# Kernel optimization log

Measured on AMD Instinct MI355X. Metric: run time of the kernel, lower is better.

## Reference

```python
import jax, jax.numpy as jnp
import numpy as np

N_HEADS = 16

def _rope_tables(L, head_dim, dtype):
    inv_freq = 1.0 / (10000.0 ** (jnp.arange(0, head_dim, 2, dtype=jnp.float32) / head_dim))
    t = jnp.arange(L, dtype=jnp.float32)
    freqs = jnp.outer(t, inv_freq)            # [L, head_dim/2]
    emb = jnp.concatenate([freqs, freqs], -1)  # [L, head_dim]
    return jnp.cos(emb).astype(dtype), jnp.sin(emb).astype(dtype)

def _apply_rope(x, cos, sin):
    # x: [B, L, H, hd]; cos/sin: [1, L, 1, hd]
    half = x.shape[-1] // 2
    x1, x2 = x[..., :half], x[..., half:]
    x_rot = jnp.concatenate([-x2, x1], -1)
    return x * cos + x_rot * sin

def setup_inputs() -> dict:
    key = jax.random.key(0)
    ks = jax.random.split(key, 5)
    D = 1024
    s = 0.02
    return {
        "x": jax.random.normal(ks[0], (4, 2048, D), jnp.float32),
        "w_qkv": jax.random.normal(ks[1], (3 * D, D), jnp.float32) * s,
        "b_qkv": jax.random.normal(ks[2], (3 * D,), jnp.float32) * s,
        "w_out": jax.random.normal(ks[3], (D, D), jnp.float32) * s,
        "b_out": jax.random.normal(ks[4], (D,), jnp.float32) * s,
    }

def reference(x, w_qkv, b_qkv, w_out, b_out):
    B, L, D = x.shape
    H = N_HEADS
    hd = D // H
    scale = hd ** -0.5
    qkv = (x @ w_qkv.T + b_qkv).reshape(B, L, 3, H, hd)
    q, k, v = qkv[:, :, 0], qkv[:, :, 1], qkv[:, :, 2]  # [B,L,H,hd]
    cos, sin = _rope_tables(L, hd, x.dtype)
    cos = cos[None, :, None, :]
    sin = sin[None, :, None, :]
    q = _apply_rope(q, cos, sin)
    k = _apply_rope(k, cos, sin)
    # [B,H,L,L] scores, non-causal softmax
    attn = jnp.einsum('blhd,bmhd->bhlm', q, k) * scale
    attn = jax.nn.softmax(attn, axis=-1)
    out = jnp.einsum('bhlm,bmhd->blhd', attn, v).reshape(B, L, D)
    return out @ w_out.T + b_out
```

## Files before the change

kernel.cpp:

```cpp
#include <hip/hip_runtime.h>
#include <stdint.h>

typedef __attribute__((ext_vector_type(4))) float f32x4;
typedef __attribute__((ext_vector_type(8))) short bf16x8;
typedef __attribute__((ext_vector_type(4))) short s16x4;
typedef __attribute__((ext_vector_type(4))) float fp32x4;

#define QSCALE 0.18033688f

__device__ __forceinline__ short f2bf(float f) {
    union { float f; unsigned u; } v; v.f = f;
    unsigned u = v.u;
    unsigned r = u + 0x7fffu + ((u >> 16) & 1u);
    return (short)(r >> 16);
}
__device__ __forceinline__ unsigned cvtpk(float a, float b) {
    unsigned r;
    asm("v_cvt_pk_bf16_f32 %0, %1, %2" : "=v"(r) : "v"(a), "v"(b));
    return r;
}

__device__ __forceinline__ void gld_lds16(const void* g, void* l) {
    __builtin_amdgcn_global_load_lds(
        (const __attribute__((address_space(1))) unsigned int*)(uintptr_t)g,
        (__attribute__((address_space(3))) unsigned int*)(uintptr_t)l,
        16, 0, 0);
}

__global__ __launch_bounds__(256) void cast_kernel(const float* __restrict__ in,
                                                   short* __restrict__ out, int n) {
    int idx = (blockIdx.x * 256 + threadIdx.x) * 8;
    if (idx >= n) return;
    fp32x4 a = *(const fp32x4*)&in[idx];
    fp32x4 b = *(const fp32x4*)&in[idx + 4];
    union { unsigned w[4]; bf16x8 v; } u;
    u.w[0] = cvtpk(a[0], a[1]); u.w[1] = cvtpk(a[2], a[3]);
    u.w[2] = cvtpk(b[0], b[1]); u.w[3] = cvtpk(b[2], b[3]);
    *(bf16x8*)&out[idx] = u.v;
}

__global__ __launch_bounds__(256) void rope_table_kernel(float* __restrict__ tab) {
    int idx = blockIdx.x * 256 + threadIdx.x;
    int l = idx >> 5, d = idx & 31;
    float inv = expf(-(float)d / 32.f * logf(10000.f));
    float ang = (float)l * inv;
    tab[idx * 2 + 0] = cosf(ang);
    tab[idx * 2 + 1] = sinf(ang);
}

template<int MODE>
__global__ __launch_bounds__(256) void gemm_bt(const short* __restrict__ A,
                                               const short* __restrict__ B,
                                               const float* __restrict__ bias,
                                               void* __restrict__ Cout,
                                               short* __restrict__ VTout,
                                               const float* __restrict__ tab,
                                               int M, int N, int K) {
    __shared__ short As[128 * 64];
    __shared__ short Bs[128 * 64];
    const int tid = threadIdx.x;
    const int lane = tid & 63, wave = tid >> 6;
    const int i15 = lane & 15, g = lane >> 4;
    const int wr = wave >> 1, wc = wave & 1;
    const int m0 = blockIdx.y * 128, n0 = blockIdx.x * 128;

    const int xr3 = i15 & 3, xb2 = (i15 >> 2) & 1;
    const int cLo = g ^ xr3;
    const int aoff0 = (wr * 64 + i15) * 64 + (xb2 * 4 + cLo) * 8;
    const int aoff1 = (wr * 64 + i15) * 64 + ((1 ^ xb2) * 4 + cLo) * 8;
    const int boff0 = (wc * 64 + i15) * 64 + (xb2 * 4 + cLo) * 8;
    const int boff1 = (wc * 64 + i15) * 64 + ((1 ^ xb2) * 4 + cLo) * 8;

    f32x4 acc[4][4] = {};

    for (int k0 = 0; k0 < K; k0 += 64) {
        __syncthreads();
#pragma unroll
        for (int r = 0; r < 4; ++r) {
            const int gx = r * 256 + tid;
            const int row = gx >> 3, s = gx & 7;
            const int ss = s ^ (row & 7);
            gld_lds16(A + (size_t)(m0 + row) * K + k0 + ss * 8,
                      As + (size_t)(r * 256 + wave * 64) * 8);
            gld_lds16(B + (size_t)(n0 + row) * K + k0 + ss * 8,
                      Bs + (size_t)(r * 256 + wave * 64) * 8);
        }
        __syncthreads();
#pragma unroll
        for (int ks = 0; ks < 2; ++ks) {
            const int ao = ks ? aoff1 : aoff0, bo = ks ? boff1 : boff0;
            bf16x8 af[4], bfr[4];
#pragma unroll
            for (int m = 0; m < 4; ++m) af[m] = *(const bf16x8*)&As[ao + m * 1024];
#pragma unroll
            for (int n = 0; n < 4; ++n) bfr[n] = *(const bf16x8*)&Bs[bo + n * 1024];
#pragma unroll
            for (int m = 0; m < 4; ++m)
#pragma unroll
                for (int n = 0; n < 4; ++n)
                    acc[m][n] = __builtin_amdgcn_mfma_f32_16x16x32_bf16(af[m], bfr[n], acc[m][n], 0, 0, 0);
        }
    }

    if (MODE == 0) {
#pragma unroll
        for (int m = 0; m < 4; ++m)
#pragma unroll
            for (int n = 0; n < 4; ++n) {
                int col = n0 + wc * 64 + n * 16 + i15;
                float bcol = bias[col];
#pragma unroll
                for (int j = 0; j < 4; ++j) {
                    int row = m0 + wr * 64 + m * 16 + g * 4 + j;
                    ((float*)Cout)[(size_t)row * N + col] = acc[m][n][j] + bcol;
                }
            }
    } else {
        const int sec = n0 >> 10;
        if (sec < 2) {
            const float qs = (sec == 0) ? QSCALE : 1.0f;
            short* out = (short*)Cout;
#pragma unroll
            for (int m = 0; m < 4; ++m) {
#pragma unroll
                for (int pp = 0; pp < 2; ++pp) {
                    int d = pp * 16 + i15;
                    int collo = n0 + wc * 64 + pp * 16 + i15;
                    float blo = bias[collo], bhi = bias[collo + 32];
#pragma unroll
                    for (int j = 0; j < 4; ++j) {
                        int row = m0 + wr * 64 + m * 16 + g * 4 + j;
                        int l = row & 2047;
                        float2 cs = *(const float2*)&tab[(l * 32 + d) * 2];
                        float x1 = acc[m][pp][j] + blo;
                        float x2 = acc[m][pp + 2][j] + bhi;
                        out[(size_t)row * 3072 + collo]      = f2bf((x1 * cs.x - x2 * cs.y) * qs);
                        out[(size_t)row * 3072 + collo + 32] = f2bf((x2 * cs.x + x1 * cs.y) * qs);
                    }
                }
            }
        } else {
#pragma unroll
            for (int m = 0; m < 4; ++m) {
                int rbase = m0 + wr * 64 + m * 16 + g * 4;
                int lbase = rbase & 2047, bidx = rbase >> 11;
#pragma unroll
                for (int n = 0; n < 4; ++n) {
                    int vcol = (n0 - 2048) + wc * 64 + n * 16 + i15;
                    int h = vcol >> 6, d = vcol & 63;
                    float bb = bias[n0 + wc * 64 + n * 16 + i15];
                    union { unsigned w[2]; s16x4 v; } u;
                    u.w[0] = cvtpk(acc[m][n][0] + bb, acc[m][n][1] + bb);
                    u.w[1] = cvtpk(acc[m][n][2] + bb, acc[m][n][3] + bb);
                    *(s16x4*)&VTout[((size_t)(bidx * 16 + h) * 64 + d) * 2048 + lbase] = u.v;
                }
            }
        }
    }
}

__global__ __launch_bounds__(512, 8) void attn_kernel(const short* __restrict__ qkv,
                                                      const short* __restrict__ VT,
                                                      short* __restrict__ O) {
    __shared__ short Ks[2][64 * 64];
    __shared__ short Vs[2][64 * 64];
    int orig = blockIdx.x;
    int xcd = orig & 7, idx = orig >> 3;
    int bh = xcd * 8 + (idx >> 4), qt = idx & 15;
    int b = bh >> 4, h = bh & 15;
    int tid = threadIdx.x, lane = tid & 63, wave = tid >> 6;
    int i15 = lane & 15, g = lane >> 4;
    int q0 = qt * 128;

    size_t qrow = (size_t)(b * 2048 + q0 + wave * 16 + i15);
    bf16x8 qf[2];
    qf[0] = *(const bf16x8*)&qkv[qrow * 3072 + h * 64 + 0  + g * 8];
    qf[1] = *(const bf16x8*)&qkv[qrow * 3072 + h * 64 + 32 + g * 8];

    bf16x8 onesf;
#pragma unroll
    for (int e = 0; e < 8; ++e) onesf[e] = (short)0x3F80;

    {
    }
    const int srow = tid >> 3, ss8 = (tid & 7) ^ (srow & 7);
    const int sprow = (srow & 0x23) | ((srow & 0x10) >> 2) | ((srow & 0x0C) << 1);
    const short* kp = qkv + (size_t)(b * 2048) * 3072 + 1024 + h * 64
                      + (size_t)sprow * 3072 + ss8 * 8;
    const short* vp = VT + (size_t)bh * 64 * 2048 + (size_t)srow * 2048 + ss8 * 8;

    const int xr3 = i15 & 3, xb2 = (i15 >> 2) & 1;
    const int cLo = g ^ xr3;
    const int o0 = i15 * 64 + (xb2 * 4 + cLo) * 8;
    const int o1 = i15 * 64 + ((1 ^ xb2) * 4 + cLo) * 8;

    f32x4 acc_o[4] = {};
    f32x4 acc_l = {0.f, 0.f, 0.f, 0.f};

#define STAGE(bk, bv)                                        \
    do {                                                     \
        gld_lds16(kp, (bk) + wave * 512);                    \
        gld_lds16(vp, (bv) + wave * 512);                    \
        kp += 64 * 3072;                                     \
        vp += 64;                                            \
    } while (0)

    STAGE(Ks[0], Vs[0]);

    for (int t = 0; t < 32; ++t) {
        const int cur = t & 1;
        if (t > 0) {
            __builtin_amdgcn_s_barrier();
            __builtin_amdgcn_sched_barrier(0);
        }
        if (t + 1 < 32) {
            STAGE(Ks[cur ^ 1], Vs[cur ^ 1]);
            asm volatile("s_waitcnt vmcnt(2)" ::: "memory");
        } else {
            asm volatile("s_waitcnt vmcnt(0)" ::: "memory");
        }
        __builtin_amdgcn_s_barrier();
        __builtin_amdgcn_sched_barrier(0);

        const short* ks = Ks[cur];
        const short* vs = Vs[cur];

        f32x4 sa[4] = {};
        __builtin_amdgcn_s_setprio(1);
#pragma unroll
        for (int kb = 0; kb < 2; ++kb) {
            const int ko = kb ? o1 : o0;
#pragma unroll
            for (int jb = 0; jb < 4; ++jb) {
                bf16x8 kf = *(const bf16x8*)&ks[ko + jb * 1024];
                sa[jb] = __builtin_amdgcn_mfma_f32_16x16x32_bf16(kf, qf[kb], sa[jb], 0, 0, 0);
            }
        }
        __builtin_amdgcn_s_setprio(0);

        float p[4][4];
#pragma unroll
        for (int jb = 0; jb < 4; ++jb)
#pragma unroll
            for (int r = 0; r < 4; ++r)
                p[jb][r] = __builtin_amdgcn_exp2f(sa[jb][r]);

        bf16x8 pf[2];
#pragma unroll
        for (int kb = 0; kb < 2; ++kb) {
            union { unsigned w[4]; bf16x8 v; } u;
            u.w[0] = cvtpk(p[2 * kb][0],     p[2 * kb][1]);
            u.w[1] = cvtpk(p[2 * kb][2],     p[2 * kb][3]);
            u.w[2] = cvtpk(p[2 * kb + 1][0], p[2 * kb + 1][1]);
            u.w[3] = cvtpk(p[2 * kb + 1][2], p[2 * kb + 1][3]);
            pf[kb] = u.v;
        }

        __builtin_amdgcn_s_setprio(1);
#pragma unroll
        for (int db = 0; db < 4; ++db) {
#pragma unroll
            for (int kb = 0; kb < 2; ++kb) {
                bf16x8 vf = *(const bf16x8*)&vs[(kb ? o1 : o0) + db * 1024];
                acc_o[db] = __builtin_amdgcn_mfma_f32_16x16x32_bf16(pf[kb], vf, acc_o[db], 0, 0, 0);
            }
        }
        acc_l = __builtin_amdgcn_mfma_f32_16x16x32_bf16(pf[0], onesf, acc_l, 0, 0, 0);
        acc_l = __builtin_amdgcn_mfma_f32_16x16x32_bf16(pf[1], onesf, acc_l, 0, 0, 0);
        __builtin_amdgcn_s_setprio(0);
    }
#undef STAGE

    float linv4[4];
#pragma unroll
    for (int r = 0; r < 4; ++r) linv4[r] = 1.f / acc_l[r];
#pragma unroll
    for (int db = 0; db < 4; ++db) {
        int ocol = h * 64 + db * 16 + i15;
#pragma unroll
        for (int r = 0; r < 4; ++r) {
            int orow = b * 2048 + q0 + wave * 16 + g * 4 + r;
            O[(size_t)orow * 1024 + ocol] = f2bf(acc_o[db][r] * linv4[r]);
        }
    }
}

extern "C" void kernel_launch(void* const* d_in, const int* in_sizes, int n_in,
                              void* d_out, int out_size, void* d_ws, size_t ws_size,
                              hipStream_t stream) {
    const float* x     = (const float*)d_in[0];
    const float* w_qkv = (const float*)d_in[1];
    const float* b_qkv = (const float*)d_in[2];
    const float* w_out = (const float*)d_in[3];
    const float* b_out = (const float*)d_in[4];

    char* ws = (char*)d_ws;
    short* qkvb = (short*)(ws);
    short* xb   = (short*)(ws + 50331648);
    short* wqb  = (short*)(ws + 67108864);
    short* wob  = (short*)(ws + 73400320);
    short* VT   = (short*)(ws + 75497472);
    float* rt   = (float*)(ws + 92274688);
    short* Ob   = xb;

    cast_kernel<<<4096, 256, 0, stream>>>(x, xb, 8388608);
    cast_kernel<<<1536, 256, 0, stream>>>(w_qkv, wqb, 3145728);
    cast_kernel<<<512, 256, 0, stream>>>(w_out, wob, 1048576);
    rope_table_kernel<<<256, 256, 0, stream>>>(rt);

    gemm_bt<1><<<dim3(24, 64), 256, 0, stream>>>(xb, wqb, b_qkv, qkvb, VT, rt, 8192, 3072, 1024);
    attn_kernel<<<1024, 512, 0, stream>>>(qkvb, VT, Ob);
    gemm_bt<0><<<dim3(8, 64), 256, 0, stream>>>(Ob, wob, b_out, d_out, nullptr, nullptr, 8192, 1024, 1024);
}
```

Before: 192.2 us.

## Pipeline GEMM with triple-buffered LDS, 256x128 tiles, and XCD-aware block swizzle

Rewrites the bf16 GEMM main loop to use a three-slot LDS ring with asynchronous global-to-LDS prefetch two tiles ahead. Loads are split into halves that are interleaved with MFMA phases, using s_setprio and explicit waitcnt/barriers in place of full __syncthreads around each tile. Block tiles grow to 256x128 with 512 threads, and block IDs are remapped across the 8 XCDs for cache locality. The aim is to hide global-load latency behind MFMA work and cut the number of blocks and barriers. The cost is more LDS per block (144KB), which limits occupancy, and fewer blocks, which risks tail imbalance on the small output GEMM.

```diff
diff --git a/kernel.cpp b/kernel.cpp
--- a/kernel.cpp
+++ b/kernel.cpp
@@ -49,20 +49,25 @@
 }
 
 template<int MODE>
-__global__ __launch_bounds__(256) void gemm_bt(const short* __restrict__ A,
-                                               const short* __restrict__ B,
-                                               const float* __restrict__ bias,
-                                               void* __restrict__ Cout,
-                                               short* __restrict__ VTout,
-                                               const float* __restrict__ tab,
-                                               int M, int N, int K) {
-    __shared__ short As[128 * 64];
-    __shared__ short Bs[128 * 64];
+__global__ __launch_bounds__(512, 2) void gemm_bt(const short* __restrict__ A,
+                                                  const short* __restrict__ B,
+                                                  const float* __restrict__ bias,
+                                                  void* __restrict__ Cout,
+                                                  short* __restrict__ VTout,
+                                                  const float* __restrict__ tab,
+                                                  int M, int N, int K) {
+    __shared__ short lds[3 * 24576];
     const int tid = threadIdx.x;
     const int lane = tid & 63, wave = tid >> 6;
     const int i15 = lane & 15, g = lane >> 4;
     const int wr = wave >> 1, wc = wave & 1;
-    const int m0 = blockIdx.y * 128, n0 = blockIdx.x * 128;
+
+    const int nbx = gridDim.x;
+    const int nwg = nbx * gridDim.y;
+    int bid = blockIdx.y * nbx + blockIdx.x;
+    int sw = (bid & 7) * (nwg >> 3) + (bid >> 3);
+    const int m0 = (sw / nbx) * 256;
+    const int n0 = (sw % nbx) * 128;
 
     const int xr3 = i15 & 3, xb2 = (i15 >> 2) & 1;
     const int cLo = g ^ xr3;
@@ -71,36 +76,87 @@
     const int boff0 = (wc * 64 + i15) * 64 + (xb2 * 4 + cLo) * 8;
     const int boff1 = (wc * 64 + i15) * 64 + ((1 ^ xb2) * 4 + cLo) * 8;
 
+    const int srow = tid >> 3;
+    const int ss = (tid & 7) ^ (srow & 7);
+    const short* a0 = A + (size_t)(m0 + srow) * K + ss * 8;
+    const short* a1 = a0 + (size_t)64 * K;
+    const short* a2 = a0 + (size_t)128 * K;
+    const short* a3 = a0 + (size_t)192 * K;
+    const short* b0 = B + (size_t)(n0 + srow) * K + ss * 8;
+    const short* b1 = b0 + (size_t)64 * K;
+
+#define ST_A(slot, r, p) do { gld_lds16(p, lds + (slot) * 24576 + ((r) * 512 + wave * 64) * 8); p += 64; } while (0)
+#define ST_B(slot, r, p) do { gld_lds16(p, lds + (slot) * 24576 + 16384 + ((r) * 512 + wave * 64) * 8); p += 64; } while (0)
+
+    ST_A(0, 0, a0); ST_A(0, 1, a1); ST_B(0, 0, b0);
+    ST_A(0, 2, a2); ST_A(0, 3, a3); ST_B(0, 1, b1);
+    ST_A(1, 0, a0); ST_A(1, 1, a1); ST_B(1, 0, b0);
+    ST_A(1, 2, a2); ST_A(1, 3, a3); ST_B(1, 1, b1);
+
     f32x4 acc[4][4] = {};
-
-    for (int k0 = 0; k0 < K; k0 += 64) {
-        __syncthreads();
-#pragma unroll
-        for (int r = 0; r < 4; ++r) {
-            const int gx = r * 256 + tid;
-            const int row = gx >> 3, s = gx & 7;
-            const int ss = s ^ (row & 7);
-            gld_lds16(A + (size_t)(m0 + row) * K + k0 + ss * 8,
-                      As + (size_t)(r * 256 + wave * 64) * 8);
-            gld_lds16(B + (size_t)(n0 + row) * K + k0 + ss * 8,
-                      Bs + (size_t)(r * 256 + wave * 64) * 8);
-        }
-        __syncthreads();
-#pragma unroll
-        for (int ks = 0; ks < 2; ++ks) {
-            const int ao = ks ? aoff1 : aoff0, bo = ks ? boff1 : boff0;
-            bf16x8 af[4], bfr[4];
-#pragma unroll
-            for (int m = 0; m < 4; ++m) af[m] = *(const bf16x8*)&As[ao + m * 1024];
-#pragma unroll
-            for (int n = 0; n < 4; ++n) bfr[n] = *(const bf16x8*)&Bs[bo + n * 1024];
-#pragma unroll
-            for (int m = 0; m < 4; ++m)
-#pragma unroll
-                for (int n = 0; n < 4; ++n)
-                    acc[m][n] = __builtin_amdgcn_mfma_f32_16x16x32_bf16(af[m], bfr[n], acc[m][n], 0, 0, 0);
-        }
+    const int NT = K >> 6;
+    int slc = 0;
+
+    for (int t = 0; t < NT; ++t) {
+        int sl2 = slc + 2; if (sl2 >= 3) sl2 -= 3;
+        if (t == NT - 1) asm volatile("s_waitcnt vmcnt(0)" ::: "memory");
+        else             asm volatile("s_waitcnt vmcnt(6)" ::: "memory");
+        __builtin_amdgcn_s_barrier();
+        __builtin_amdgcn_sched_barrier(0);
+
+        const short* As_ = lds + slc * 24576;
+        const short* Bs_ = As_ + 16384;
+        const bool pre = (t + 2 < NT);
+
+        if (pre) { ST_A(sl2, 0, a0); ST_A(sl2, 1, a1); ST_B(sl2, 0, b0); }
+        bf16x8 af[4][2], bfr[2][2];
+#pragma unroll
+        for (int m = 0; m < 4; ++m) {
+            af[m][0] = *(const bf16x8*)&As_[aoff0 + m * 1024];
+            af[m][1] = *(const bf16x8*)&As_[aoff1 + m * 1024];
+        }
+#pragma unroll
+        for (int n = 0; n < 2; ++n) {
+            bfr[n][0] = *(const bf16x8*)&Bs_[boff0 + n * 1024];
+            bfr[n][1] = *(const bf16x8*)&Bs_[boff1 + n * 1024];
+        }
+        __builtin_amdgcn_s_barrier();
+        asm volatile("s_waitcnt lgkmcnt(0)" ::: "memory");
+        __builtin_amdgcn_sched_barrier(0);
+        __builtin_amdgcn_s_setprio(1);
+#pragma unroll
+        for (int m = 0; m < 4; ++m)
+#pragma unroll
+            for (int n = 0; n < 2; ++n)
+#pragma unroll
+                for (int ks = 0; ks < 2; ++ks)
+                    acc[m][n] = __builtin_amdgcn_mfma_f32_16x16x32_bf16(af[m][ks], bfr[n][ks], acc[m][n], 0, 0, 0);
+        __builtin_amdgcn_s_setprio(0);
+
+        if (pre) { ST_A(sl2, 2, a2); ST_A(sl2, 3, a3); ST_B(sl2, 1, b1); }
+        bf16x8 bfr2[2][2];
+#pragma unroll
+        for (int n = 0; n < 2; ++n) {
+            bfr2[n][0] = *(const bf16x8*)&Bs_[boff0 + (n + 2) * 1024];
+            bfr2[n][1] = *(const bf16x8*)&Bs_[boff1 + (n + 2) * 1024];
+        }
+        __builtin_amdgcn_s_barrier();
+        asm volatile("s_waitcnt lgkmcnt(0)" ::: "memory");
+        __builtin_amdgcn_sched_barrier(0);
+        __builtin_amdgcn_s_setprio(1);
+#pragma unroll
+        for (int m = 0; m < 4; ++m)
+#pragma unroll
+            for (int n = 0; n < 2; ++n)
+#pragma unroll
+                for (int ks = 0; ks < 2; ++ks)
+                    acc[m][n + 2] = __builtin_amdgcn_mfma_f32_16x16x32_bf16(af[m][ks], bfr2[n][ks], acc[m][n + 2], 0, 0, 0);
+        __builtin_amdgcn_s_setprio(0);
+
+        slc = (slc == 2) ? 0 : slc + 1;
     }
+#undef ST_A
+#undef ST_B
 
     if (MODE == 0) {
 #pragma unroll
@@ -181,8 +237,6 @@
 #pragma unroll
     for (int e = 0; e < 8; ++e) onesf[e] = (short)0x3F80;
 
-    {
-    }
     const int srow = tid >> 3, ss8 = (tid & 7) ^ (srow & 7);
     const int sprow = (srow & 0x23) | ((srow & 0x10) >> 2) | ((srow & 0x0C) << 1);
     const short* kp = qkv + (size_t)(b * 2048) * 3072 + 1024 + h * 64
@@ -308,7 +362,7 @@
     cast_kernel<<<512, 256, 0, stream>>>(w_out, wob, 1048576);
     rope_table_kernel<<<256, 256, 0, stream>>>(rt);
 
-    gemm_bt<1><<<dim3(24, 64), 256, 0, stream>>>(xb, wqb, b_qkv, qkvb, VT, rt, 8192, 3072, 1024);
+    gemm_bt<1><<<dim3(24, 32), 512, 0, stream>>>(xb, wqb, b_qkv, qkvb, VT, rt, 8192, 3072, 1024);
     attn_kernel<<<1024, 512, 0, stream>>>(qkvb, VT, Ob);
-    gemm_bt<0><<<dim3(8, 64), 256, 0, stream>>>(Ob, wob, b_out, d_out, nullptr, nullptr, 8192, 1024, 1024);
-}
+    gemm_bt<0><<<dim3(8, 32), 512, 0, stream>>>(Ob, wob, b_out, d_out, nullptr, nullptr, 8192, 1024, 1024);
+}
```

Result: faster. 175.7 us (-8.6%).
